# Kernel tuning notes

Hardware: AMD Instinct MI355X
Metric: run time of the kernel (lower is better)

## Reference

```python
import jax, jax.numpy as jnp
import numpy as np

HIDDEN = 2048
NH = 32
NKV = 8
HD = HIDDEN // NH  # 64
GROUP = NH // NKV  # 4


def setup_inputs() -> dict:
    key = jax.random.key(0)
    ks = jax.random.split(key, 9)
    s = 1.0 / np.sqrt(HIDDEN)
    x = jax.random.normal(ks[0], (2, 2048, HIDDEN), dtype=jnp.float32)
    Wq = jax.random.uniform(ks[1], (HIDDEN, HIDDEN), jnp.float32, -s, s)
    bq = jax.random.uniform(ks[2], (HIDDEN,), jnp.float32, -s, s)
    Wk = jax.random.uniform(ks[3], (HIDDEN, NKV * HD), jnp.float32, -s, s)
    bk = jax.random.uniform(ks[4], (NKV * HD,), jnp.float32, -s, s)
    Wv = jax.random.uniform(ks[5], (HIDDEN, NKV * HD), jnp.float32, -s, s)
    bv = jax.random.uniform(ks[6], (NKV * HD,), jnp.float32, -s, s)
    Wo = jax.random.uniform(ks[7], (HIDDEN, HIDDEN), jnp.float32, -s, s)
    bo = jax.random.uniform(ks[8], (HIDDEN,), jnp.float32, -s, s)
    return {"x": x, "Wq": Wq, "bq": bq, "Wk": Wk, "bk": bk,
            "Wv": Wv, "bv": bv, "Wo": Wo, "bo": bo}


def reference(x, Wq, bq, Wk, bk, Wv, bv, Wo, bo):
    B, S, D = x.shape
    scale = 1.0 / np.sqrt(HD).astype(np.float32)
    q = (x @ Wq + bq).reshape(B, S, NH, HD).transpose(0, 2, 1, 3)   # [B,H,S,hd]
    k = (x @ Wk + bk).reshape(B, S, NKV, HD).transpose(0, 2, 1, 3)  # [B,KV,S,hd]
    v = (x @ Wv + bv).reshape(B, S, NKV, HD).transpose(0, 2, 1, 3)
    # repeat_interleave KV heads: kv head j serves query heads j*GROUP..(j+1)*GROUP-1
    k = jnp.repeat(k, GROUP, axis=1)  # [B,H,S,hd]
    v = jnp.repeat(v, GROUP, axis=1)
    scores = jnp.einsum('bhqd,bhkd->bhqk', q, k) * scale  # [B,H,S,S]
    w = jax.nn.softmax(scores, axis=-1)
    out = jnp.einsum('bhqk,bhkd->bhqd', w, v)              # [B,H,S,hd]
    out = out.transpose(0, 2, 1, 3).reshape(B, S, D)
    return out @ Wo + bo
```

## Files before the change

kernel.cpp:

```cpp
#include <hip/hip_runtime.h>

#define HID 2048
#define SEQ 2048
#define NH_ 32
#define NKV_ 8
#define HD_ 64

typedef __attribute__((ext_vector_type(8))) short s8v;
typedef __attribute__((ext_vector_type(4))) float f4v;
typedef __attribute__((ext_vector_type(4))) unsigned int u4v;
typedef unsigned int u32;
typedef unsigned short u16;

#define QSCALE 0.18033688011112042f

__device__ __forceinline__ u16 f2bf(float f) {
  u32 u = __builtin_bit_cast(u32, f);
  u = u + 0x7FFFu + ((u >> 16) & 1u);
  return (u16)(u >> 16);
}

__device__ __forceinline__ float hw_exp2(float x) {
  float r;
  asm("v_exp_f32 %0, %1" : "=v"(r) : "v"(x));
  return r;
}

__device__ __forceinline__ void gl_lds16(const void* g, void* l) {
  __builtin_amdgcn_global_load_lds((const __attribute__((address_space(1))) u32*)g,
                                   (__attribute__((address_space(3))) u32*)l, 16, 0, 0);
}

__device__ __forceinline__ void transp_body(const float* __restrict__ W,
                                            u16* __restrict__ Wt, int K, int N,
                                            int bx, int by, int tid) {
  __shared__ float t[64][65];
  const int n0 = bx * 64, k0 = by * 64;
  const int tr = tid >> 4, tc = tid & 15;
#pragma unroll
  for (int i = 0; i < 4; ++i) {
    int r = i * 16 + tr;
    const float4 v = *reinterpret_cast<const float4*>(&W[(size_t)(k0 + r) * N + n0 + tc * 4]);
    t[r][tc * 4 + 0] = v.x; t[r][tc * 4 + 1] = v.y;
    t[r][tc * 4 + 2] = v.z; t[r][tc * 4 + 3] = v.w;
  }
  __syncthreads();
#pragma unroll
  for (int i = 0; i < 4; ++i) {
    int r = i * 16 + tr;
    ushort4 o;
    o.x = f2bf(t[tc * 4 + 0][r]); o.y = f2bf(t[tc * 4 + 1][r]);
    o.z = f2bf(t[tc * 4 + 2][r]); o.w = f2bf(t[tc * 4 + 3][r]);
    *reinterpret_cast<ushort4*>(&Wt[(size_t)(n0 + r) * K + k0 + tc * 4]) = o;
  }
}

__global__ __launch_bounds__(256) void prep_k(const float* __restrict__ x,
                                              const float* __restrict__ Wq,
                                              const float* __restrict__ Wk,
                                              const float* __restrict__ Wv,
                                              const float* __restrict__ Wo,
                                              u16* __restrict__ xb,
                                              u16* __restrict__ wqkvt,
                                              u16* __restrict__ wot) {
  const int bid = blockIdx.x, tid = threadIdx.x;
  if (bid < 8192) {
    const int i = (bid * 256 + tid) * 4;
    const float4 v = *reinterpret_cast<const float4*>(x + i);
    ushort4 o;
    o.x = f2bf(v.x); o.y = f2bf(v.y); o.z = f2bf(v.z); o.w = f2bf(v.w);
    *reinterpret_cast<ushort4*>(xb + i) = o;
  } else if (bid < 8192 + 1024) {
    const int b2 = bid - 8192;
    transp_body(Wq, wqkvt, 2048, 2048, b2 & 31, b2 >> 5, tid);
  } else if (bid < 8192 + 1024 + 256) {
    const int b2 = bid - (8192 + 1024);
    transp_body(Wk, wqkvt + (size_t)2048 * 2048, 2048, 512, b2 & 7, b2 >> 3, tid);
  } else if (bid < 8192 + 1024 + 512) {
    const int b2 = bid - (8192 + 1024 + 256);
    transp_body(Wv, wqkvt + (size_t)2560 * 2048, 2048, 512, b2 & 7, b2 >> 3, tid);
  } else {
    const int b2 = bid - (8192 + 1024 + 512);
    transp_body(Wo, wot, 2048, 2048, b2 & 31, b2 >> 5, tid);
  }
}

template <int MODE>
__global__ __launch_bounds__(256) void gemm_k(const u16* __restrict__ A,
                                              const u16* __restrict__ Bt,
                                              const float* __restrict__ b0,
                                              const float* __restrict__ b1,
                                              const float* __restrict__ b2,
                                              void* __restrict__ o0,
                                              void* __restrict__ o1,
                                              void* __restrict__ o2,
                                              int M, int N, int K) {
  __shared__ u16 As[128 * 64];
  __shared__ u16 Bs[128 * 64];
  const int tid = threadIdx.x;
  const int w = tid >> 6, l = tid & 63;
  const int wr = w >> 1, wc = w & 1;
  const int lr = l & 15, lg = l >> 4;
  const int m0 = blockIdx.y * 128, n0 = blockIdx.x * 128;
  f4v acc[4][4] = {};
  for (int k0 = 0; k0 < K; k0 += 64) {
#pragma unroll
    for (int i = 0; i < 4; ++i) {
      int c = i * 256 + tid;
      int r = c >> 3, p = c & 7;
      gl_lds16(&A[(size_t)(m0 + r) * K + k0 + ((p ^ (r & 7)) * 8)], &As[c * 8]);
      gl_lds16(&Bt[(size_t)(n0 + r) * K + k0 + ((p ^ (r & 7)) * 8)], &Bs[c * 8]);
    }
    __syncthreads();
#pragma unroll
    for (int kc = 0; kc < 2; ++kc) {
      s8v af[4], bf[4];
#pragma unroll
      for (int m = 0; m < 4; ++m)
        af[m] = *reinterpret_cast<const s8v*>(
            &As[(wr * 64 + m * 16 + lr) * 64 + ((((kc << 2) + lg) ^ (lr & 7)) << 3)]);
#pragma unroll
      for (int n = 0; n < 4; ++n)
        bf[n] = *reinterpret_cast<const s8v*>(
            &Bs[(wc * 64 + n * 16 + lr) * 64 + ((((kc << 2) + lg) ^ (lr & 7)) << 3)]);
#pragma unroll
      for (int m = 0; m < 4; ++m)
#pragma unroll
        for (int n = 0; n < 4; ++n)
          acc[m][n] = __builtin_amdgcn_mfma_f32_16x16x32_bf16(af[m], bf[n], acc[m][n], 0, 0, 0);
    }
    __syncthreads();
  }
#pragma unroll
  for (int n = 0; n < 4; ++n) {
    const int col = n0 + wc * 64 + n * 16 + lr;
    float bb, scl = 1.0f;
    if (MODE == 2) {
      bb = b0[col];
    } else {
      if (col < 2048) { bb = b0[col]; scl = QSCALE; }
      else if (col < 2560) { bb = b1[col - 2048]; }
      else { bb = b2[col - 2560]; }
    }
#pragma unroll
    for (int m = 0; m < 4; ++m) {
#pragma unroll
      for (int r = 0; r < 4; ++r) {
        const int row = m0 + wr * 64 + m * 16 + lg * 4 + r;
        const float v = (acc[m][n][r] + bb) * scl;
        if (MODE == 2) {
          ((float*)o0)[(size_t)row * N + col] = v;
        } else {
          const int b = row >> 11, s = row & (SEQ - 1);
          if (col < 2048) {
            const int h = col >> 6, d = col & 63;
            ((u16*)o0)[((((size_t)b * NH_ + h) * SEQ + s) << 6) + d] = f2bf(v);
          } else if (col < 2560) {
            const int kv = (col - 2048) >> 6, d = (col - 2048) & 63;
            ((u16*)o1)[((((size_t)b * NKV_ + kv) * SEQ + s) << 6) + d] = f2bf(v);
          } else {
            const int kv = (col - 2560) >> 6, d = (col - 2560) & 63;
            const int sp = (s & ~31) | (((s >> 2) & 3) << 3) | (((s >> 4) & 1) << 2) | (s & 3);
            ((u16*)o2)[(((size_t)b * NKV_ + kv) * HD_ + d) * SEQ + sp] = f2bf(v);
          }
        }
      }
    }
  }
}

__global__ __launch_bounds__(256) void attn_k(const u16* __restrict__ Q,
                                              const u16* __restrict__ Kg,
                                              const u16* __restrict__ Vt,
                                              u16* __restrict__ Og) {
  __shared__ u16 Ks[128 * 64];
  __shared__ u16 Vs[64 * 128];
  const int tid = threadIdx.x;
  const int w = tid >> 6, l = tid & 63;
  const int lr = l & 15, lg = l >> 4;
  const int qt = blockIdx.x, h = blockIdx.y, b = blockIdx.z;
  const int kvh = h >> 2;
  const u16* Qp = Q + ((((size_t)b * NH_ + h) * SEQ + qt * 128) << 6);
  const u16* Kp = Kg + (((size_t)b * NKV_ + kvh) * SEQ << 6);
  const u16* Vp = Vt + ((size_t)b * NKV_ + kvh) * HD_ * SEQ;

  s8v qf[2][2];
#pragma unroll
  for (int i = 0; i < 2; ++i)
#pragma unroll
    for (int kc = 0; kc < 2; ++kc)
      qf[i][kc] = *reinterpret_cast<const s8v*>(
          &Qp[(w * 32 + i * 16 + lr) * 64 + kc * 32 + lg * 8]);

  float ps[2] = {0.f, 0.f};
  f4v Oacc[2][4] = {};

#define STAGE_K(KT)                                                              \
  {                                                                              \
    _Pragma("unroll") for (int i_ = 0; i_ < 4; ++i_) {                           \
      int c_ = i_ * 256 + tid;                                                   \
      int r_ = c_ >> 3, p_ = c_ & 7;                                             \
      gl_lds16(&Kp[((size_t)((KT) * 128 + r_)) * 64 + ((p_ ^ (r_ & 7)) * 8)],    \
               &Ks[c_ * 8]);                                                     \
    }                                                                            \
  }
#define STAGE_V(KT)                                                              \
  {                                                                              \
    _Pragma("unroll") for (int i_ = 0; i_ < 4; ++i_) {                           \
      int c_ = i_ * 256 + tid;                                                   \
      int r_ = c_ >> 4, p_ = c_ & 15;                                            \
      gl_lds16(&Vp[(size_t)r_ * SEQ + (KT) * 128 + ((p_ ^ (r_ & 15)) * 8)],      \
               &Vs[c_ * 8]);                                                     \
    }                                                                            \
  }

  STAGE_K(0);
  STAGE_V(0);
  __syncthreads();

  const int NT = SEQ / 128;
  for (int kt = 0; kt < NT; ++kt) {
    f4v sc[2][8] = {};
#pragma unroll
    for (int kb = 0; kb < 8; ++kb) {
      const int rk = kb * 16 + lr;
#pragma unroll
      for (int kc = 0; kc < 2; ++kc) {
        s8v kfr = *reinterpret_cast<const s8v*>(
            &Ks[rk * 64 + ((((kc << 2) + lg) ^ (lr & 7)) << 3)]);
#pragma unroll
        for (int i = 0; i < 2; ++i)
          sc[i][kb] = __builtin_amdgcn_mfma_f32_16x16x32_bf16(kfr, qf[i][kc], sc[i][kb], 0, 0, 0);
      }
    }

    __syncthreads();
    if (kt + 1 < NT) STAGE_K(kt + 1);

#pragma unroll
    for (int i = 0; i < 2; ++i) {
      float s = 0.f;
#pragma unroll
      for (int kb = 0; kb < 8; ++kb)
#pragma unroll
        for (int r = 0; r < 4; ++r) {
          const float e = hw_exp2(sc[i][kb][r]);
          sc[i][kb][r] = e;
          s += e;
        }
      ps[i] += s;
    }

#pragma unroll
    for (int c = 0; c < 4; ++c) {
      s8v pa[2];
#pragma unroll
      for (int i = 0; i < 2; ++i) {
        u32 d0, d1, d2, d3;
        asm("v_cvt_pk_bf16_f32 %0, %1, %2" : "=v"(d0) : "v"(sc[i][2 * c][0]), "v"(sc[i][2 * c][1]));
        asm("v_cvt_pk_bf16_f32 %0, %1, %2" : "=v"(d1) : "v"(sc[i][2 * c][2]), "v"(sc[i][2 * c][3]));
        asm("v_cvt_pk_bf16_f32 %0, %1, %2" : "=v"(d2) : "v"(sc[i][2 * c + 1][0]), "v"(sc[i][2 * c + 1][1]));
        asm("v_cvt_pk_bf16_f32 %0, %1, %2" : "=v"(d3) : "v"(sc[i][2 * c + 1][2]), "v"(sc[i][2 * c + 1][3]));
        u4v t = {d0, d1, d2, d3};
        pa[i] = __builtin_bit_cast(s8v, t);
      }
#pragma unroll
      for (int df = 0; df < 4; ++df) {
        const int d = df * 16 + lr;
        const int ch = ((c << 2) + lg) ^ lr;
        const s8v vb = *reinterpret_cast<const s8v*>(&Vs[d * 128 + (ch << 3)]);
#pragma unroll
        for (int i = 0; i < 2; ++i)
          Oacc[i][df] = __builtin_amdgcn_mfma_f32_16x16x32_bf16(pa[i], vb, Oacc[i][df], 0, 0, 0);
      }
    }

    __syncthreads();
    if (kt + 1 < NT) STAGE_V(kt + 1);
  }

#pragma unroll
  for (int i = 0; i < 2; ++i) {
    ps[i] += __shfl_xor(ps[i], 16);
    ps[i] += __shfl_xor(ps[i], 32);
  }
  const int sbase = qt * 128 + w * 32;
#pragma unroll
  for (int i = 0; i < 2; ++i)
#pragma unroll
    for (int r = 0; r < 4; ++r) {
      const float linv = 1.0f / __shfl(ps[i], (lg << 2) + r);
      const int srow = sbase + i * 16 + lg * 4 + r;
#pragma unroll
      for (int df = 0; df < 4; ++df)
        Og[((size_t)b * SEQ + srow) * HID + h * 64 + df * 16 + lr] =
            f2bf(Oacc[i][df][r] * linv);
    }
#undef STAGE_K
#undef STAGE_V
}

extern "C" void kernel_launch(void* const* d_in, const int* in_sizes, int n_in,
                              void* d_out, int out_size, void* d_ws, size_t ws_size,
                              hipStream_t stream) {
  (void)in_sizes; (void)n_in; (void)out_size;
  const float* x  = (const float*)d_in[0];
  const float* Wq = (const float*)d_in[1];
  const float* bq = (const float*)d_in[2];
  const float* Wk = (const float*)d_in[3];
  const float* bk = (const float*)d_in[4];
  const float* Wv = (const float*)d_in[5];
  const float* bv = (const float*)d_in[6];
  const float* Wo = (const float*)d_in[7];
  const float* bo = (const float*)d_in[8];
  float* out = (float*)d_out;

  u16* ws    = (u16*)d_ws;
  u16* xb    = ws;
  u16* wqkvt = xb + 8388608;
  u16* wot   = wqkvt + 6291456;
  u16* qb    = wot + 4194304;
  u16* kbuf  = qb + 8388608;
  u16* vtb   = kbuf + 2097152;
  u16* ab    = vtb + 2097152;
  if (ws_size < (size_t)(8388608 + 6291456 + 4194304 + 8388608 + 2097152 +
                         2097152 + 8388608) * 2) return;

  prep_k<<<10752, 256, 0, stream>>>(x, Wq, Wk, Wv, Wo, xb, wqkvt, wot);

  gemm_k<3><<<dim3(24, 32), 256, 0, stream>>>(xb, wqkvt, bq, bk, bv,
                                              qb, kbuf, vtb, 4096, 3072, 2048);

  attn_k<<<dim3(16, 32, 2), 256, 0, stream>>>(qb, kbuf, vtb, ab);

  gemm_k<2><<<dim3(16, 32), 256, 0, stream>>>(ab, wot, bo, nullptr, nullptr,
                                              out, nullptr, nullptr, 4096, 2048, 2048);
}
```

Before: 211.3 us.

## Swizzle block order for L2 locality and compute softmax denominator via MFMA

Remaps workgroup IDs in both the GEMM and attention kernels with a stride-8 swizzle, so that concurrently scheduled blocks share operand tiles and KV heads in cache. In attention, the per-row sum of exponentials is no longer accumulated with VALU adds and cross-lane shuffles. It is computed by an extra MFMA of the bf16 probabilities against a ones vector. This moves reduction work onto the matrix units and removes the shuffle epilogue. The denominator now sums the bf16-rounded probabilities, which matches the values used in P·V.

```diff
diff --git a/kernel.cpp b/kernel.cpp
--- a/kernel.cpp
+++ b/kernel.cpp
@@ -101,7 +101,11 @@
   const int w = tid >> 6, l = tid & 63;
   const int wr = w >> 1, wc = w & 1;
   const int lr = l & 15, lg = l >> 4;
-  const int m0 = blockIdx.y * 128, n0 = blockIdx.x * 128;
+  const int gx = gridDim.x;
+  const int nwg = gx * gridDim.y;
+  const int lin = blockIdx.x + gx * blockIdx.y;
+  const int swz = (lin & 7) * (nwg >> 3) + (lin >> 3);
+  const int m0 = (swz / gx) * 128, n0 = (swz % gx) * 128;
   f4v acc[4][4] = {};
   for (int k0 = 0; k0 < K; k0 += 64) {
 #pragma unroll
@@ -178,7 +182,9 @@
   const int tid = threadIdx.x;
   const int w = tid >> 6, l = tid & 63;
   const int lr = l & 15, lg = l >> 4;
-  const int qt = blockIdx.x, h = blockIdx.y, b = blockIdx.z;
+  const int lin = blockIdx.x + 16 * (blockIdx.y + 32 * blockIdx.z);
+  const int swz = ((lin & 7) << 7) | (lin >> 3);
+  const int qt = swz & 15, h = (swz >> 4) & 31, b = swz >> 9;
   const int kvh = h >> 2;
   const u16* Qp = Q + ((((size_t)b * NH_ + h) * SEQ + qt * 128) << 6);
   const u16* Kp = Kg + (((size_t)b * NKV_ + kvh) * SEQ << 6);
@@ -192,8 +198,11 @@
       qf[i][kc] = *reinterpret_cast<const s8v*>(
           &Qp[(w * 32 + i * 16 + lr) * 64 + kc * 32 + lg * 8]);
 
-  float ps[2] = {0.f, 0.f};
+  const u4v ones_u = {0x3F803F80u, 0x3F803F80u, 0x3F803F80u, 0x3F803F80u};
+  const s8v ones8 = __builtin_bit_cast(s8v, ones_u);
+
   f4v Oacc[2][4] = {};
+  f4v den[2] = {};
 
 #define STAGE_K(KT)                                                              \
   {                                                                              \
@@ -238,18 +247,12 @@
     if (kt + 1 < NT) STAGE_K(kt + 1);
 
 #pragma unroll
-    for (int i = 0; i < 2; ++i) {
-      float s = 0.f;
+    for (int i = 0; i < 2; ++i)
 #pragma unroll
       for (int kb = 0; kb < 8; ++kb)
 #pragma unroll
-        for (int r = 0; r < 4; ++r) {
-          const float e = hw_exp2(sc[i][kb][r]);
-          sc[i][kb][r] = e;
-          s += e;
-        }
-      ps[i] += s;
-    }
+        for (int r = 0; r < 4; ++r)
+          sc[i][kb][r] = hw_exp2(sc[i][kb][r]);
 
 #pragma unroll
     for (int c = 0; c < 4; ++c) {
@@ -263,6 +266,7 @@
         asm("v_cvt_pk_bf16_f32 %0, %1, %2" : "=v"(d3) : "v"(sc[i][2 * c + 1][2]), "v"(sc[i][2 * c + 1][3]));
         u4v t = {d0, d1, d2, d3};
         pa[i] = __builtin_bit_cast(s8v, t);
+        den[i] = __builtin_amdgcn_mfma_f32_16x16x32_bf16(pa[i], ones8, den[i], 0, 0, 0);
       }
 #pragma unroll
       for (int df = 0; df < 4; ++df) {
@@ -279,17 +283,12 @@
     if (kt + 1 < NT) STAGE_V(kt + 1);
   }
 
-#pragma unroll
-  for (int i = 0; i < 2; ++i) {
-    ps[i] += __shfl_xor(ps[i], 16);
-    ps[i] += __shfl_xor(ps[i], 32);
-  }
   const int sbase = qt * 128 + w * 32;
 #pragma unroll
   for (int i = 0; i < 2; ++i)
 #pragma unroll
     for (int r = 0; r < 4; ++r) {
-      const float linv = 1.0f / __shfl(ps[i], (lg << 2) + r);
+      const float linv = 1.0f / den[i][r];
       const int srow = sbase + i * 16 + lg * 4 + r;
 #pragma unroll
       for (int df = 0; df < 4; ++df)
```

After: 209.6 us. Within noise of the previous version (-0.8%).
